# Kernel optimization log

Hardware: AMD Instinct MI355X
Metric: run time of the kernel (lower is better)

The kernel has to match this reference:

```python
import jax, jax.numpy as jnp
jax.config.update("jax_enable_x64", True)
import numpy as np

N_E = 8192      # codebook size
E_DIM = 512     # code dim
BETA = 0.25
SK_EPS = 0.003
SK_ITERS = 5
N_TOK = 8192


def sinkhorn(d, eps, iters):
    # d: [B, K] centered distances in float64 (matches torch .double())
    Q = jnp.exp(-d / eps).T            # [K, B]
    K, B = Q.shape
    Q = Q / Q.sum()

    def body(Q, _):
        Q = Q / Q.sum(axis=1, keepdims=True) / K   # normalize rows (codes)
        Q = Q / Q.sum(axis=0, keepdims=True) / B   # normalize cols (tokens)
        return Q, None

    Q, _ = jax.lax.scan(body, Q, None, length=iters)
    Q = Q * B
    return Q.T                          # [B, K]


def setup_inputs() -> dict:
    key = jax.random.key(0)
    k1, k2 = jax.random.split(key)
    x = jax.random.normal(k1, (N_TOK, E_DIM), dtype=jnp.float32)
    # nn.Embedding weight init: uniform(-1/n_e, 1/n_e)
    emb = jax.random.uniform(k2, (N_E, E_DIM), dtype=jnp.float32,
                             minval=-1.0 / N_E, maxval=1.0 / N_E)
    return {"x": x, "emb": emb}


def reference(x, emb):
    latent = x.reshape(-1, E_DIM)                                  # [B, D]
    # pairwise squared L2: ||z||^2 + ||e||^2 - 2 z e^T  -> [B, K]
    d = (jnp.sum(latent ** 2, axis=1, keepdims=True)
         + jnp.sum(emb ** 2, axis=1)[None, :]
         - 2.0 * latent @ emb.T)
    # center_distance_for_constraint
    mx = d.max()
    mn = d.min()
    middle = (mx + mn) / 2
    amplitude = mx - middle + 1e-5
    dc = ((d - middle) / amplitude).astype(jnp.float64)
    Q = sinkhorn(dc, SK_EPS, SK_ITERS)
    indices = jnp.argmax(Q, axis=-1)                               # [B]
    x_q = emb[indices].reshape(x.shape)
    codebook_loss = jnp.mean((x_q - jax.lax.stop_gradient(x)) ** 2)
    commitment_loss = jnp.mean((jax.lax.stop_gradient(x_q) - x) ** 2)
    loss = codebook_loss + BETA * commitment_loss
    # straight-through estimator
    x_q_st = x + jax.lax.stop_gradient(x_q - x)
    return x_q_st, loss, indices.reshape(x.shape[:-1])
```

## Files before the change

kernel.cpp:

```cpp
#include <hip/hip_runtime.h>
#include <cfloat>
#include <cstdint>
#include <cstddef>

#define NTOK 8192
#define NE   8192
#define DIM  512
#define OUT0 4194304

__device__ __forceinline__ double fexp_d(double x){
  const double L2E = 1.4426950408889634074;
  const double LN2 = 0.69314718055994530942;
  double kd = rint(x * L2E);
  double r  = fma(-kd, LN2, x);
  double p = 2.4801587301587301566e-05;
  p = fma(p, r, 1.9841269841269841253e-04);
  p = fma(p, r, 1.3888888888888889419e-03);
  p = fma(p, r, 8.3333333333333332177e-03);
  p = fma(p, r, 4.1666666666666664354e-02);
  p = fma(p, r, 1.6666666666666665741e-01);
  p = fma(p, r, 5.0e-01);
  p = fma(p, r, 1.0);
  p = fma(p, r, 1.0);
  long long eb = ((long long)(1023 + (int)kd)) << 52;
  return p * __longlong_as_double(eb);
}

__device__ __forceinline__ unsigned int f2ord(float f){
  unsigned int u = __float_as_uint(f);
  return (u & 0x80000000u) ? ~u : (u | 0x80000000u);
}
__device__ __forceinline__ float ord2f(unsigned int v){
  unsigned int u = (v & 0x80000000u) ? (v ^ 0x80000000u) : ~v;
  return __uint_as_float(u);
}

__device__ float pw128_sq(const float* __restrict__ p){
  float r[8];
#pragma unroll
  for (int j = 0; j < 8; ++j) r[j] = __fmul_rn(p[j], p[j]);
#pragma unroll
  for (int i = 8; i < 128; i += 8)
#pragma unroll
    for (int j = 0; j < 8; ++j) r[j] = __fadd_rn(r[j], __fmul_rn(p[i+j], p[i+j]));
  float s01 = __fadd_rn(r[0], r[1]), s23 = __fadd_rn(r[2], r[3]);
  float s45 = __fadd_rn(r[4], r[5]), s67 = __fadd_rn(r[6], r[7]);
  return __fadd_rn(__fadd_rn(s01, s23), __fadd_rn(s45, s67));
}
__device__ float pw512_sq(const float* __restrict__ p){
  float s0 = __fadd_rn(pw128_sq(p),       pw128_sq(p + 128));
  float s1 = __fadd_rn(pw128_sq(p + 256), pw128_sq(p + 384));
  return __fadd_rn(s0, s1);
}

__global__ __launch_bounds__(256) void normsK(const float* __restrict__ X, const float* __restrict__ E,
    float* __restrict__ avec, float* __restrict__ hvec){
  int blk = blockIdx.x;
  int i = (blk & 31) * 256 + threadIdx.x;
  if (blk < 32) avec[i] = pw512_sq(X + (size_t)i * DIM);
  else          hvec[i] = pw512_sq(E + (size_t)i * DIM);
}

__global__ void initK(unsigned int* sc32){
  if (threadIdx.x == 0){ sc32[0] = 0u; sc32[1] = 0xFFFFFFFFu; }
}

__global__ void finalizeK(const unsigned int* sc32, float* scf){
  if (threadIdx.x == 0){
    float mx = ord2f(sc32[0]);
    float mn = ord2f(sc32[1]);
    float middle = __fmul_rn(__fadd_rn(mx, mn), 0.5f);
    float amp    = __fadd_rn(__fsub_rn(mx, middle), 1e-5f);
    scf[0] = middle; scf[1] = amp;
  }
}

__global__ void diagK(float* __restrict__ out, int n, float tag){
  int i = blockIdx.x * blockDim.x + threadIdx.x;
  int stride = gridDim.x * blockDim.x;
  for (; i < n; i += stride) out[i] = (i == OUT0) ? tag : 0.f;
}

#define GBM 128
#define GBN 128
#define GBK 32
#define GLDT 132
__global__ __launch_bounds__(256, 4) void gemm128(const float* __restrict__ X, const float* __restrict__ E,
    const float* __restrict__ avec, const float* __restrict__ hvec,
    float* __restrict__ dmat, unsigned int* __restrict__ sc32){
  __shared__ float As[GBK][GLDT];
  __shared__ float Bs[GBK][GLDT];
  __shared__ float red[256];
  int tid = threadIdx.x;
  int tx = tid & 15, ty = tid >> 4;
  int bm = blockIdx.y * GBM, bn = blockIdx.x * GBN;

  float acc[2][4][2][4];
#pragma unroll
  for (int ih = 0; ih < 2; ++ih)
#pragma unroll
    for (int i = 0; i < 4; ++i)
#pragma unroll
      for (int jh = 0; jh < 2; ++jh)
#pragma unroll
        for (int j = 0; j < 4; ++j) acc[ih][i][jh][j] = 0.f;

  for (int kt = 0; kt < DIM; kt += GBK){
#pragma unroll
    for (int s = 0; s < 4; ++s){
      int flat = tid + s * 256;
      int m  = flat >> 3;
      int k4 = (flat & 7) * 4;
      float4 va = *(const float4*)(X + (size_t)(bm + m) * DIM + kt + k4);
      As[k4+0][m] = va.x; As[k4+1][m] = va.y; As[k4+2][m] = va.z; As[k4+3][m] = va.w;
      float4 vb = *(const float4*)(E + (size_t)(bn + m) * DIM + kt + k4);
      Bs[k4+0][m] = vb.x; Bs[k4+1][m] = vb.y; Bs[k4+2][m] = vb.z; Bs[k4+3][m] = vb.w;
    }
    __syncthreads();
#pragma unroll
    for (int kk = 0; kk < GBK; ++kk){
      float a[2][4], b[2][4];
      *(float4*)a[0] = *(const float4*)&As[kk][ty * 4];
      *(float4*)a[1] = *(const float4*)&As[kk][64 + ty * 4];
      *(float4*)b[0] = *(const float4*)&Bs[kk][tx * 4];
      *(float4*)b[1] = *(const float4*)&Bs[kk][64 + tx * 4];
#pragma unroll
      for (int ih = 0; ih < 2; ++ih)
#pragma unroll
        for (int i = 0; i < 4; ++i)
#pragma unroll
          for (int jh = 0; jh < 2; ++jh)
#pragma unroll
            for (int j = 0; j < 4; ++j)
              acc[ih][i][jh][j] = fmaf(a[ih][i], b[jh][j], acc[ih][i][jh][j]);
    }
    __syncthreads();
  }

  float lmax = -FLT_MAX, lmin = FLT_MAX;
#pragma unroll
  for (int ih = 0; ih < 2; ++ih){
#pragma unroll
    for (int i = 0; i < 4; ++i){
      int gr = bm + ih * 64 + ty * 4 + i;
      float a = avec[gr];
#pragma unroll
      for (int jh = 0; jh < 2; ++jh){
        float dv[4];
#pragma unroll
        for (int j = 0; j < 4; ++j){
          int gc = bn + jh * 64 + tx * 4 + j;
          float t = __fadd_rn(a, hvec[gc]);
          float d = __fsub_rn(t, 2.0f * acc[ih][i][jh][j]);
          dv[j] = d;
          lmax = fmaxf(lmax, d); lmin = fminf(lmin, d);
        }
        *(float4*)(dmat + (size_t)gr * NE + bn + jh * 64 + tx * 4) = *(float4*)&dv[0];
      }
    }
  }
  red[tid] = lmax; __syncthreads();
  for (int s = 128; s > 0; s >>= 1){ if (tid < s) red[tid] = fmaxf(red[tid], red[tid+s]); __syncthreads(); }
  float bmax = red[0];
  __syncthreads();
  red[tid] = lmin; __syncthreads();
  for (int s = 128; s > 0; s >>= 1){ if (tid < s) red[tid] = fminf(red[tid], red[tid+s]); __syncthreads(); }
  if (tid == 0){
    atomicMax(&sc32[0], f2ord(bmax));
    atomicMin(&sc32[1], f2ord(red[0]));
  }
}

#define EXPD(x) fexp_d((double)__fdiv_rn(__fsub_rn((x), middle), amp) * NIE)

__global__ __launch_bounds__(256) void rowPassK(const float* __restrict__ dmat, const double* __restrict__ wvec,
    const float* __restrict__ scf, double* __restrict__ partials){
  int tid = threadIdx.x;
  int k0 = blockIdx.x * 1024 + tid * 4;
  int b0 = blockIdx.y * 256;
  float middle = scf[0], amp = scf[1];
  const double NIE = -(1.0 / 0.003);
  const float* p = dmat + (size_t)b0 * NE + k0;
  double a0 = 0.0, a1 = 0.0, a2 = 0.0, a3 = 0.0;
  if (wvec){
    for (int bb = 0; bb < 256; bb += 2){
      float4 v0 = *(const float4*)(p + (size_t)(bb+0) * NE);
      float4 v1 = *(const float4*)(p + (size_t)(bb+1) * NE);
      double w0 = wvec[b0+bb+0], w1 = wvec[b0+bb+1];
      a0 = fma(EXPD(v0.x), w0, a0); a1 = fma(EXPD(v0.y), w0, a1);
      a2 = fma(EXPD(v0.z), w0, a2); a3 = fma(EXPD(v0.w), w0, a3);
      a0 = fma(EXPD(v1.x), w1, a0); a1 = fma(EXPD(v1.y), w1, a1);
      a2 = fma(EXPD(v1.z), w1, a2); a3 = fma(EXPD(v1.w), w1, a3);
    }
  } else {
    for (int bb = 0; bb < 256; bb += 2){
      float4 v0 = *(const float4*)(p + (size_t)(bb+0) * NE);
      float4 v1 = *(const float4*)(p + (size_t)(bb+1) * NE);
      a0 += EXPD(v0.x); a1 += EXPD(v0.y); a2 += EXPD(v0.z); a3 += EXPD(v0.w);
      a0 += EXPD(v1.x); a1 += EXPD(v1.y); a2 += EXPD(v1.z); a3 += EXPD(v1.w);
    }
  }
  double* q = partials + (size_t)blockIdx.y * NE + k0;
  q[0] = a0; q[1] = a1; q[2] = a2; q[3] = a3;
}

__global__ void reduceAK(const double* __restrict__ partials, double* __restrict__ ak){
  int k = blockIdx.x * 256 + threadIdx.x;
  double s = 0.0;
  for (int c = 0; c < 32; ++c) s += partials[(size_t)c * NE + k];
  ak[k] = 1.0 / (8192.0 * s);
}

__global__ __launch_bounds__(256) void colPassK(const float* __restrict__ dmat, const double* __restrict__ ak,
    const float* __restrict__ scf, double* __restrict__ bvec){
  __shared__ double sd[256];
  int b = blockIdx.x, tid = threadIdx.x;
  float middle = scf[0], amp = scf[1];
  const double NIE = -(1.0 / 0.003);
  const float* row = dmat + (size_t)b * NE;
  double acc = 0.0;
  for (int kb = 0; kb < 32; kb += 4){
    int k0 = tid + (kb+0) * 256, k1 = tid + (kb+1) * 256, k2 = tid + (kb+2) * 256, k3 = tid + (kb+3) * 256;
    float r0 = row[k0], r1 = row[k1], r2 = row[k2], r3 = row[k3];
    double q0 = ak[k0], q1 = ak[k1], q2 = ak[k2], q3 = ak[k3];
    acc = fma(EXPD(r0), q0, acc);
    acc = fma(EXPD(r1), q1, acc);
    acc = fma(EXPD(r2), q2, acc);
    acc = fma(EXPD(r3), q3, acc);
  }
  sd[tid] = acc; __syncthreads();
  for (int s = 128; s > 0; s >>= 1){ if (tid < s) sd[tid] += sd[tid+s]; __syncthreads(); }
  if (tid == 0) bvec[b] = 1.0 / (8192.0 * sd[0]);
}

__global__ void lnaK(const double* __restrict__ ak, double* __restrict__ lna){
  int k = blockIdx.x * 256 + threadIdx.x;
  lna[k] = log(ak[k]);
}

__global__ __launch_bounds__(256) void argmaxLossK(const float* __restrict__ dmat, const double* __restrict__ lna,
    const float* __restrict__ scf, const float* __restrict__ X, const float* __restrict__ E,
    float* __restrict__ idxF, double* __restrict__ lparts){
  __shared__ double sv[256];
  __shared__ int    si[256];
  __shared__ int    sidx;
  int b = blockIdx.x, tid = threadIdx.x;
  float middle = scf[0], amp = scf[1];
  const double NIE = -(1.0 / 0.003);
  const float* row = dmat + (size_t)b * NE;
  double best = -1.0e300; int bk = NE;
#pragma unroll 2
  for (int c = 0; c < 8; ++c){
    int k = c * 1024 + tid * 4;
    float4 v = *(const float4*)(row + k);
    double l0 = lna[k], l1 = lna[k+1], l2 = lna[k+2], l3 = lna[k+3];
    double t0 = fma((double)__fdiv_rn(__fsub_rn(v.x, middle), amp), NIE, l0);
    double t1 = fma((double)__fdiv_rn(__fsub_rn(v.y, middle), amp), NIE, l1);
    double t2 = fma((double)__fdiv_rn(__fsub_rn(v.z, middle), amp), NIE, l2);
    double t3 = fma((double)__fdiv_rn(__fsub_rn(v.w, middle), amp), NIE, l3);
    if (t0 > best){ best = t0; bk = k; }
    if (t1 > best){ best = t1; bk = k+1; }
    if (t2 > best){ best = t2; bk = k+2; }
    if (t3 > best){ best = t3; bk = k+3; }
  }
  sv[tid] = best; si[tid] = bk; __syncthreads();
  for (int s = 128; s > 0; s >>= 1){
    if (tid < s){
      double o = sv[tid+s]; int ok = si[tid+s];
      if (o > sv[tid] || (o == sv[tid] && ok < si[tid])){ sv[tid] = o; si[tid] = ok; }
    }
    __syncthreads();
  }
  if (tid == 0){ idxF[b] = (float)si[0]; sidx = si[0]; }
  __syncthreads();

  int id = sidx;
  const float* xr = X + (size_t)b * DIM;
  const float* er = E + (size_t)id * DIM;
  double ls = 0.0;
#pragma unroll
  for (int c = 0; c < 2; ++c){
    int dpos = tid + c * 256;
    float diff = __fsub_rn(er[dpos], xr[dpos]);
    ls = fma((double)diff, (double)diff, ls);
  }
  sv[tid] = ls; __syncthreads();
  for (int s = 128; s > 0; s >>= 1){ if (tid < s) sv[tid] += sv[tid+s]; __syncthreads(); }
  if (tid == 0) lparts[b] = sv[0];
}

__global__ __launch_bounds__(256) void lossFinK(const double* __restrict__ lparts, float* __restrict__ lossOut){
  __shared__ double sd[256];
  int tid = threadIdx.x;
  double s = 0.0;
  for (int b = tid; b < NTOK; b += 256) s += lparts[b];
  sd[tid] = s; __syncthreads();
  for (int st = 128; st > 0; st >>= 1){ if (tid < st) sd[tid] += sd[tid+st]; __syncthreads(); }
  if (tid == 0){
    double v = sd[0] / (double)((size_t)NTOK * DIM);
    float vf = (float)v;
    lossOut[0] = __fadd_rn(vf, __fmul_rn(0.25f, vf));
  }
}

__global__ __launch_bounds__(256) void out0K(const float* __restrict__ X, const float* __restrict__ E,
    const float* __restrict__ idxF, float* __restrict__ out0){
  int b = blockIdx.x, tid = threadIdx.x;
  int id = (int)idxF[b];
  const float* xr = X + (size_t)b * DIM;
  const float* er = E + (size_t)id * DIM;
#pragma unroll
  for (int c = 0; c < 2; ++c){
    int dpos = tid + c * 256;
    float xv = xr[dpos];
    float diff = __fsub_rn(er[dpos], xv);
    out0[(size_t)b * DIM + dpos] = __fadd_rn(xv, diff);
  }
}

extern "C" void kernel_launch(void* const* d_in, const int* in_sizes, int n_in,
                              void* d_out, int out_size, void* d_ws, size_t ws_size,
                              hipStream_t stream){
  (void)in_sizes; (void)n_in;
  const float* X = (const float*)d_in[0];
  const float* E = (const float*)d_in[1];
  float* out = (float*)d_out;

  if (ws_size < 268435456ull || d_ws == nullptr){
    diagK<<<2048, 256, 0, stream>>>(out, out_size, (float)(ws_size >> 20));
    return;
  }
  float* dmat = (float*)d_ws;

  float*  avec   = out;
  float*  hvec   = out + 8192;
  double* parts  = (double*)(out + 16384);
  double* ak     = (double*)(out + 540672);
  double* bvec   = (double*)(out + 557056);
  double* lna    = (double*)(out + 573440);
  unsigned int* sc32 = (unsigned int*)(out + 589824);
  float*  scf    = out + 589826;
  double* lparts = parts;

  float* out0    = out;
  float* lossOut = out + OUT0;
  float* idxF    = out + OUT0 + 1;

  initK<<<1, 64, 0, stream>>>(sc32);
  normsK<<<64, 256, 0, stream>>>(X, E, avec, hvec);

  dim3 gg(NE / GBN, NTOK / GBM);
  gemm128<<<gg, 256, 0, stream>>>(X, E, avec, hvec, dmat, sc32);
  finalizeK<<<1, 64, 0, stream>>>(sc32, scf);

  dim3 rp(8, 32);
  rowPassK<<<rp, 256, 0, stream>>>(dmat, nullptr, scf, parts);
  reduceAK<<<32, 256, 0, stream>>>(parts, ak);
  for (int it = 0; it < 4; ++it){
    colPassK<<<NTOK, 256, 0, stream>>>(dmat, ak, scf, bvec);
    rowPassK<<<rp, 256, 0, stream>>>(dmat, bvec, scf, parts);
    reduceAK<<<32, 256, 0, stream>>>(parts, ak);
  }

  lnaK<<<32, 256, 0, stream>>>(ak, lna);
  argmaxLossK<<<NTOK, 256, 0, stream>>>(dmat, lna, scf, X, E, idxF, lparts);
  lossFinK<<<1, 256, 0, stream>>>(lparts, lossOut);
  out0K<<<NTOK, 256, 0, stream>>>(X, E, idxF, out0);
}
```

Measured before the change: 1.638 ms.

## Widen GEMM tile, split row-pass over more blocks, add colPass accumulators

The GEMM tile becomes 128x256 with a K step of 16, so each thread computes 128 outputs and the B operand is reused more per shared-memory load. The row pass now splits tokens into 128 chunks of 64 instead of 32 chunks of 256, giving more blocks to hide latency, and reduceAK sums 128 partials. The column pass uses four independent double accumulators to break the FMA dependency chain. The scratch pointers in the output buffer move to fit the larger partials array. Costs are higher register pressure in the GEMM (occupancy hint drops to 2) and more partial traffic for the reduction.

```diff
diff --git a/kernel.cpp b/kernel.cpp
--- a/kernel.cpp
+++ b/kernel.cpp
@@ -82,54 +82,62 @@
 }
 
 #define GBM 128
-#define GBN 128
-#define GBK 32
-#define GLDT 132
-__global__ __launch_bounds__(256, 4) void gemm128(const float* __restrict__ X, const float* __restrict__ E,
+#define GBN 256
+#define GBK 16
+#define LDA 132
+#define LDB 260
+__global__ __launch_bounds__(256, 2) void gemm128(const float* __restrict__ X, const float* __restrict__ E,
     const float* __restrict__ avec, const float* __restrict__ hvec,
     float* __restrict__ dmat, unsigned int* __restrict__ sc32){
-  __shared__ float As[GBK][GLDT];
-  __shared__ float Bs[GBK][GLDT];
+  __shared__ float As[GBK][LDA];
+  __shared__ float Bs[GBK][LDB];
   __shared__ float red[256];
   int tid = threadIdx.x;
   int tx = tid & 15, ty = tid >> 4;
   int bm = blockIdx.y * GBM, bn = blockIdx.x * GBN;
 
-  float acc[2][4][2][4];
+  float acc[2][4][4][4];
 #pragma unroll
   for (int ih = 0; ih < 2; ++ih)
 #pragma unroll
     for (int i = 0; i < 4; ++i)
 #pragma unroll
-      for (int jh = 0; jh < 2; ++jh)
+      for (int jh = 0; jh < 4; ++jh)
 #pragma unroll
         for (int j = 0; j < 4; ++j) acc[ih][i][jh][j] = 0.f;
 
   for (int kt = 0; kt < DIM; kt += GBK){
+#pragma unroll
+    for (int s = 0; s < 2; ++s){
+      int flat = tid + s * 256;
+      int m  = flat >> 2;
+      int k4 = (flat & 3) * 4;
+      float4 va = *(const float4*)(X + (size_t)(bm + m) * DIM + kt + k4);
+      As[k4+0][m] = va.x; As[k4+1][m] = va.y; As[k4+2][m] = va.z; As[k4+3][m] = va.w;
+    }
 #pragma unroll
     for (int s = 0; s < 4; ++s){
       int flat = tid + s * 256;
-      int m  = flat >> 3;
-      int k4 = (flat & 7) * 4;
-      float4 va = *(const float4*)(X + (size_t)(bm + m) * DIM + kt + k4);
-      As[k4+0][m] = va.x; As[k4+1][m] = va.y; As[k4+2][m] = va.z; As[k4+3][m] = va.w;
+      int m  = flat >> 2;
+      int k4 = (flat & 3) * 4;
       float4 vb = *(const float4*)(E + (size_t)(bn + m) * DIM + kt + k4);
       Bs[k4+0][m] = vb.x; Bs[k4+1][m] = vb.y; Bs[k4+2][m] = vb.z; Bs[k4+3][m] = vb.w;
     }
     __syncthreads();
 #pragma unroll
     for (int kk = 0; kk < GBK; ++kk){
-      float a[2][4], b[2][4];
+      float a[2][4], b[4][4];
       *(float4*)a[0] = *(const float4*)&As[kk][ty * 4];
       *(float4*)a[1] = *(const float4*)&As[kk][64 + ty * 4];
-      *(float4*)b[0] = *(const float4*)&Bs[kk][tx * 4];
-      *(float4*)b[1] = *(const float4*)&Bs[kk][64 + tx * 4];
+#pragma unroll
+      for (int jh = 0; jh < 4; ++jh)
+        *(float4*)b[jh] = *(const float4*)&Bs[kk][jh * 64 + tx * 4];
 #pragma unroll
       for (int ih = 0; ih < 2; ++ih)
 #pragma unroll
         for (int i = 0; i < 4; ++i)
 #pragma unroll
-          for (int jh = 0; jh < 2; ++jh)
+          for (int jh = 0; jh < 4; ++jh)
 #pragma unroll
             for (int j = 0; j < 4; ++j)
               acc[ih][i][jh][j] = fmaf(a[ih][i], b[jh][j], acc[ih][i][jh][j]);
@@ -145,7 +153,7 @@
       int gr = bm + ih * 64 + ty * 4 + i;
       float a = avec[gr];
 #pragma unroll
-      for (int jh = 0; jh < 2; ++jh){
+      for (int jh = 0; jh < 4; ++jh){
         float dv[4];
 #pragma unroll
         for (int j = 0; j < 4; ++j){
@@ -176,14 +184,14 @@
 __global__ __launch_bounds__(256) void rowPassK(const float* __restrict__ dmat, const double* __restrict__ wvec,
     const float* __restrict__ scf, double* __restrict__ partials){
   int tid = threadIdx.x;
-  int k0 = blockIdx.x * 1024 + tid * 4;
-  int b0 = blockIdx.y * 256;
+  int k0 = (blockIdx.x * 256 + tid) * 4;
+  int b0 = blockIdx.y * 64;
   float middle = scf[0], amp = scf[1];
   const double NIE = -(1.0 / 0.003);
   const float* p = dmat + (size_t)b0 * NE + k0;
   double a0 = 0.0, a1 = 0.0, a2 = 0.0, a3 = 0.0;
   if (wvec){
-    for (int bb = 0; bb < 256; bb += 2){
+    for (int bb = 0; bb < 64; bb += 2){
       float4 v0 = *(const float4*)(p + (size_t)(bb+0) * NE);
       float4 v1 = *(const float4*)(p + (size_t)(bb+1) * NE);
       double w0 = wvec[b0+bb+0], w1 = wvec[b0+bb+1];
@@ -193,7 +201,7 @@
       a2 = fma(EXPD(v1.z), w1, a2); a3 = fma(EXPD(v1.w), w1, a3);
     }
   } else {
-    for (int bb = 0; bb < 256; bb += 2){
+    for (int bb = 0; bb < 64; bb += 2){
       float4 v0 = *(const float4*)(p + (size_t)(bb+0) * NE);
       float4 v1 = *(const float4*)(p + (size_t)(bb+1) * NE);
       a0 += EXPD(v0.x); a1 += EXPD(v0.y); a2 += EXPD(v0.z); a3 += EXPD(v0.w);
@@ -207,7 +215,7 @@
 __global__ void reduceAK(const double* __restrict__ partials, double* __restrict__ ak){
   int k = blockIdx.x * 256 + threadIdx.x;
   double s = 0.0;
-  for (int c = 0; c < 32; ++c) s += partials[(size_t)c * NE + k];
+  for (int c = 0; c < 128; ++c) s += partials[(size_t)c * NE + k];
   ak[k] = 1.0 / (8192.0 * s);
 }
 
@@ -218,17 +226,17 @@
   float middle = scf[0], amp = scf[1];
   const double NIE = -(1.0 / 0.003);
   const float* row = dmat + (size_t)b * NE;
-  double acc = 0.0;
+  double c0 = 0.0, c1 = 0.0, c2 = 0.0, c3 = 0.0;
   for (int kb = 0; kb < 32; kb += 4){
     int k0 = tid + (kb+0) * 256, k1 = tid + (kb+1) * 256, k2 = tid + (kb+2) * 256, k3 = tid + (kb+3) * 256;
     float r0 = row[k0], r1 = row[k1], r2 = row[k2], r3 = row[k3];
     double q0 = ak[k0], q1 = ak[k1], q2 = ak[k2], q3 = ak[k3];
-    acc = fma(EXPD(r0), q0, acc);
-    acc = fma(EXPD(r1), q1, acc);
-    acc = fma(EXPD(r2), q2, acc);
-    acc = fma(EXPD(r3), q3, acc);
-  }
-  sd[tid] = acc; __syncthreads();
+    c0 = fma(EXPD(r0), q0, c0);
+    c1 = fma(EXPD(r1), q1, c1);
+    c2 = fma(EXPD(r2), q2, c2);
+    c3 = fma(EXPD(r3), q3, c3);
+  }
+  sd[tid] = (c0 + c1) + (c2 + c3); __syncthreads();
   for (int s = 128; s > 0; s >>= 1){ if (tid < s) sd[tid] += sd[tid+s]; __syncthreads(); }
   if (tid == 0) bvec[b] = 1.0 / (8192.0 * sd[0]);
 }
@@ -335,11 +343,11 @@
   float*  avec   = out;
   float*  hvec   = out + 8192;
   double* parts  = (double*)(out + 16384);
-  double* ak     = (double*)(out + 540672);
-  double* bvec   = (double*)(out + 557056);
-  double* lna    = (double*)(out + 573440);
-  unsigned int* sc32 = (unsigned int*)(out + 589824);
-  float*  scf    = out + 589826;
+  double* ak     = (double*)(out + 2113536);
+  double* bvec   = (double*)(out + 2129920);
+  double* lna    = (double*)(out + 2146304);
+  unsigned int* sc32 = (unsigned int*)(out + 2162688);
+  float*  scf    = out + 2162690;
   double* lparts = parts;
 
   float* out0    = out;
@@ -353,7 +361,7 @@
   gemm128<<<gg, 256, 0, stream>>>(X, E, avec, hvec, dmat, sc32);
   finalizeK<<<1, 64, 0, stream>>>(sc32, scf);
 
-  dim3 rp(8, 32);
+  dim3 rp(8, 128);
   rowPassK<<<rp, 256, 0, stream>>>(dmat, nullptr, scf, parts);
   reduceAK<<<32, 256, 0, stream>>>(parts, ak);
   for (int it = 0; it < 4; ++it){
```

Result: faster. 1.531 ms (-6.5%).
